# Optimization experiments

Hardware: AMD Instinct MI355X
Metric: run time of the kernel (lower is better)

## Reference

```python
import jax, jax.numpy as jnp
import numpy as np

EPS = 1e-12  # matches torch F.normalize eps


def setup_inputs() -> dict:
    key = jax.random.key(0)
    k1, k2, k3 = jax.random.split(key, 3)
    N, C, H, W, K = 16, 1024, 32, 32, 32
    x = jax.random.normal(k1, (N, C, H, W), dtype=jnp.float32)
    # 1x1 conv weight (K, C, 1, 1) stored as (K, C)
    conv_w = jax.random.normal(k2, (K, C), dtype=jnp.float32) * 0.02
    centroids = jax.random.uniform(k3, (K, C), dtype=jnp.float32)
    return {"x": x, "conv_w": conv_w, "centroids": centroids}


def _l2norm(v, axis):
    return v / jnp.maximum(jnp.linalg.norm(v, axis=axis, keepdims=True), EPS)


def reference(x, conv_w, centroids):
    N, C, H, W = x.shape
    K = centroids.shape[0]
    # normalize_input: L2 over channel dim
    x = _l2norm(x, axis=1)
    xf = x.reshape(N, C, H * W)                      # (N, C, P)
    # 1x1 conv == per-pixel matmul -> (N, K, P)
    logits = jnp.einsum('kc,ncp->nkp', conv_w, xf)
    a = jax.nn.softmax(logits, axis=1)               # softmax over clusters
    # sum_p a[n,k,p] * (x[n,:,p] - centroids[k,:])
    # == (a @ x^T) - (sum_p a) * centroids  (two GEMMs, no (N,K,C,P) blowup)
    vlad = jnp.einsum('nkp,ncp->nkc', a, xf) - a.sum(-1)[:, :, None] * centroids[None]
    vlad = _l2norm(vlad, axis=2)                     # intra-cluster L2 norm
    vlad = vlad.reshape(N, K * C)
    vlad = _l2norm(vlad, axis=1)                     # global L2 norm
    return vlad
```

## Files before the change

kernel.cpp:

```cpp
#include <hip/hip_runtime.h>

#define NB   16
#define CC   1024
#define PP   1024
#define KK   32
#define EPSF 1e-12f

typedef __attribute__((ext_vector_type(8))) short  bf16x8;
typedef __attribute__((ext_vector_type(4))) float  f32x4;

__device__ __forceinline__ float bf2f(unsigned short u) {
    union { unsigned int i; float f; } v; v.i = ((unsigned int)u) << 16; return v.f;
}
__device__ __forceinline__ unsigned short f2bf(float f) {
    union { float f; unsigned int i; } v; v.f = f;
    return (unsigned short)((v.i + 0x7fffu + ((v.i >> 16) & 1u)) >> 16);
}

template <typename T> struct IO;
template <> struct IO<float> {
    static __device__ __forceinline__ float ld(const float* p) { return *p; }
    static __device__ __forceinline__ f32x4 ld4(const float* p) { return *(const f32x4*)p; }
    static __device__ __forceinline__ void st4(float* p, f32x4 v) { *(f32x4*)p = v; }
};
template <> struct IO<unsigned short> {
    static __device__ __forceinline__ float ld(const unsigned short* p) { return bf2f(*p); }
    static __device__ __forceinline__ f32x4 ld4(const unsigned short* p) {
        const ushort4 u = *(const ushort4*)p;
        f32x4 r; r[0] = bf2f(u.x); r[1] = bf2f(u.y); r[2] = bf2f(u.z); r[3] = bf2f(u.w);
        return r;
    }
    static __device__ __forceinline__ void st4(unsigned short* p, f32x4 v) {
        ushort4 u;
        u.x = f2bf(v[0]); u.y = f2bf(v[1]); u.z = f2bf(v[2]); u.w = f2bf(v[3]);
        *(ushort4*)p = u;
    }
};

__device__ __forceinline__ void wg_sync_fast() {
    asm volatile("s_waitcnt lgkmcnt(0)" ::: "memory");
    __builtin_amdgcn_s_barrier();
    asm volatile("" ::: "memory");
}

struct __align__(16) AttnSmem {
    unsigned short xT[2][64][72];
    unsigned short Wl[2][32][72];
    float red[16][64];
    float rn[64];
};

template <typename T>
__device__ __forceinline__ void attn_body(const T* __restrict__ x,
                                          const T* __restrict__ w,
                                          AttnSmem& sm,
                                          float* __restrict__ rnorm_ws,
                                          unsigned short* __restrict__ attn_g,
                                          float* __restrict__ asum_p) {
    const int b = blockIdx.x, t = threadIdx.x;
    const int n = b >> 4, pt = b & 15, p0 = pt * 64;
    const int lane = t & 63, wv = t >> 6;
    const int quad = lane >> 4, l15 = lane & 15;
    const int i = t >> 4;
    const int j = t & 15;
    const int wk = t >> 3;
    const int wcoff = (t & 7) * 8;
    const size_t xb = (size_t)n * CC * PP + p0;

    float ssq_t[4] = {0.f, 0.f, 0.f, 0.f};
    f32x4 acc0 = {0.f, 0.f, 0.f, 0.f}, acc1 = {0.f, 0.f, 0.f, 0.f};

    f32x4 xr[4]; f32x4 wr[2];
    #pragma unroll
    for (int r = 0; r < 4; ++r)
        xr[r] = IO<T>::ld4(&x[xb + (size_t)(4 * i + r) * PP + 4 * j]);
    wr[0] = IO<T>::ld4(&w[wk * CC + wcoff]);
    wr[1] = IO<T>::ld4(&w[wk * CC + wcoff + 4]);

    #pragma unroll
    for (int ch = 0; ch < 16; ++ch) {
        const int buf = ch & 1;
        #pragma unroll
        for (int jj = 0; jj < 4; ++jj) {
            ssq_t[jj] += xr[0][jj] * xr[0][jj] + xr[1][jj] * xr[1][jj]
                       + xr[2][jj] * xr[2][jj] + xr[3][jj] * xr[3][jj];
            ushort4 u;
            u.x = f2bf(xr[0][jj]); u.y = f2bf(xr[1][jj]);
            u.z = f2bf(xr[2][jj]); u.w = f2bf(xr[3][jj]);
            *(ushort4*)&sm.xT[buf][4 * j + jj][4 * i] = u;
        }
        {
            ushort4 u0, u1;
            u0.x = f2bf(wr[0][0]); u0.y = f2bf(wr[0][1]);
            u0.z = f2bf(wr[0][2]); u0.w = f2bf(wr[0][3]);
            u1.x = f2bf(wr[1][0]); u1.y = f2bf(wr[1][1]);
            u1.z = f2bf(wr[1][2]); u1.w = f2bf(wr[1][3]);
            *(ushort4*)&sm.Wl[buf][wk][wcoff]     = u0;
            *(ushort4*)&sm.Wl[buf][wk][wcoff + 4] = u1;
        }
        if (ch < 15) {
            const int c0 = (ch + 1) * 64;
            #pragma unroll
            for (int r = 0; r < 4; ++r)
                xr[r] = IO<T>::ld4(&x[xb + (size_t)(c0 + 4 * i + r) * PP + 4 * j]);
            wr[0] = IO<T>::ld4(&w[wk * CC + c0 + wcoff]);
            wr[1] = IO<T>::ld4(&w[wk * CC + c0 + wcoff + 4]);
        }
        wg_sync_fast();
        #pragma unroll
        for (int ks = 0; ks < 2; ++ks) {
            const bf16x8 bv  = *(const bf16x8*)&sm.xT[buf][wv * 16 + l15][ks * 32 + quad * 8];
            const bf16x8 a0  = *(const bf16x8*)&sm.Wl[buf][l15][ks * 32 + quad * 8];
            const bf16x8 a1  = *(const bf16x8*)&sm.Wl[buf][16 + l15][ks * 32 + quad * 8];
            acc0 = __builtin_amdgcn_mfma_f32_16x16x32_bf16(a0, bv, acc0, 0, 0, 0);
            acc1 = __builtin_amdgcn_mfma_f32_16x16x32_bf16(a1, bv, acc1, 0, 0, 0);
        }
    }
    #pragma unroll
    for (int jj = 0; jj < 4; ++jj) sm.red[i][4 * j + jj] = ssq_t[jj];
    __syncthreads();
    if (t < 64) {
        float ss = 0.f;
        #pragma unroll
        for (int g = 0; g < 16; ++g) ss += sm.red[g][t];
        const float rr = 1.0f / fmaxf(sqrtf(ss), EPSF);
        sm.rn[t] = rr;
        rnorm_ws[n * PP + p0 + t] = rr;
    }
    __syncthreads();
    {
        const float rr = sm.rn[wv * 16 + l15];
        float l[8];
        #pragma unroll
        for (int reg = 0; reg < 4; ++reg) { l[reg] = acc0[reg] * rr; l[4 + reg] = acc1[reg] * rr; }
        float mx = l[0];
        #pragma unroll
        for (int q = 1; q < 8; ++q) mx = fmaxf(mx, l[q]);
        mx = fmaxf(mx, __shfl_xor(mx, 16, 64));
        mx = fmaxf(mx, __shfl_xor(mx, 32, 64));
        float e[8], sum = 0.f;
        #pragma unroll
        for (int q = 0; q < 8; ++q) { e[q] = expf(l[q] - mx); sum += e[q]; }
        sum += __shfl_xor(sum, 16, 64);
        sum += __shfl_xor(sum, 32, 64);
        const float inv = 1.0f / sum;
        #pragma unroll
        for (int reg = 0; reg < 4; ++reg) {
            sm.Wl[0][quad * 4 + reg][wv * 16 + l15]      = f2bf(e[reg] * inv);
            sm.Wl[0][16 + quad * 4 + reg][wv * 16 + l15] = f2bf(e[4 + reg] * inv);
        }
    }
    __syncthreads();
    {
        const int k = t >> 3, po = (t & 7) * 8;
        const ushort4 u0 = *(const ushort4*)&sm.Wl[0][k][po];
        const ushort4 u1 = *(const ushort4*)&sm.Wl[0][k][po + 4];
        *(ushort4*)&attn_g[((size_t)n * KK + k) * PP + p0 + po]     = u0;
        *(ushort4*)&attn_g[((size_t)n * KK + k) * PP + p0 + po + 4] = u1;
        float s = bf2f(u0.x) + bf2f(u0.y) + bf2f(u0.z) + bf2f(u0.w)
                + bf2f(u1.x) + bf2f(u1.y) + bf2f(u1.z) + bf2f(u1.w);
        s += __shfl_xor(s, 1, 64);
        s += __shfl_xor(s, 2, 64);
        s += __shfl_xor(s, 4, 64);
        if ((t & 7) == 0) asum_p[(n * 16 + pt) * KK + k] = s;
    }
}

__global__ __launch_bounds__(256) void k_attn(const void* __restrict__ xv,
                                              const void* __restrict__ wv,
                                              int* __restrict__ flag,
                                              float* __restrict__ rnorm_ws,
                                              unsigned short* __restrict__ attn_g,
                                              float* __restrict__ asum_p) {
    __shared__ AttnSmem sm;
    __shared__ int s_bad;
    const int t = threadIdx.x;
    if (t == 0) s_bad = 0;
    __syncthreads();
    {
        const unsigned short* xu = (const unsigned short*)xv;
        int bad = 0;
        for (int ii = t; ii < 4096; ii += 256)
            if (((xu[ii] >> 7) & 0xFFu) > 0x9Fu) bad = 1;
        if (bad) atomicOr(&s_bad, 1);
    }
    __syncthreads();
    const int f = s_bad;
    if (blockIdx.x == 0 && t == 0) flag[0] = f;
    if (f) attn_body<float>((const float*)xv, (const float*)wv, sm, rnorm_ws, attn_g, asum_p);
    else   attn_body<unsigned short>((const unsigned short*)xv, (const unsigned short*)wv,
                                     sm, rnorm_ws, attn_g, asum_p);
}

struct VladSmem { float asum[32]; float ssq[32]; };

template <typename T>
__device__ __forceinline__ void vlad_body(const T* __restrict__ x,
                                          const T* __restrict__ cent, VladSmem& sm,
                                          const float* __restrict__ rnorm_ws,
                                          const unsigned short* __restrict__ attn_g,
                                          const float* __restrict__ asum_p,
                                          float* __restrict__ vlad,
                                          float* __restrict__ ssqnk_p) {
    const int b = blockIdx.x, t = threadIdx.x;
    const int n = b >> 5, ct = b & 31;
    const int lane = t & 63, wvi = t >> 6;
    const int quad = lane >> 4, l15 = lane & 15;
    const int mt = wvi & 1, nt = wvi >> 1;
    const int krow = mt * 16 + l15;
    const int crow = ct * 32 + nt * 16 + l15;
    if (t < 32) {
        float s = 0.f;
        #pragma unroll
        for (int ps = 0; ps < 16; ++ps) s += asum_p[(n * 16 + ps) * KK + t];
        sm.asum[t] = s;
        sm.ssq[t] = 0.f;
    }
    __syncthreads();
    const unsigned short* apq = attn_g + ((size_t)n * KK + krow) * PP + quad * 8;
    const T* xp = x + (size_t)n * CC * PP + (size_t)crow * PP + quad * 8;
    const float* rp = rnorm_ws + n * PP + quad * 8;
    f32x4 acc = {0.f, 0.f, 0.f, 0.f};
    bf16x8 avq[4]; f32x4 xq0[4], xq1[4], rq0[4], rq1[4];
    #pragma unroll
    for (int ii = 0; ii < 4; ++ii) {
        const int o = ii * 32;
        avq[ii] = *(const bf16x8*)&apq[o];
        xq0[ii] = IO<T>::ld4(&xp[o]); xq1[ii] = IO<T>::ld4(&xp[o + 4]);
        rq0[ii] = *(const f32x4*)&rp[o]; rq1[ii] = *(const f32x4*)&rp[o + 4];
    }
    #pragma unroll
    for (int st = 0; st < 32; ++st) {
        const int sl = st & 3;
        bf16x8 bv;
        #pragma unroll
        for (int jj = 0; jj < 4; ++jj) {
            bv[jj]     = (short)f2bf(xq0[sl][jj] * rq0[sl][jj]);
            bv[4 + jj] = (short)f2bf(xq1[sl][jj] * rq1[sl][jj]);
        }
        acc = __builtin_amdgcn_mfma_f32_16x16x32_bf16(avq[sl], bv, acc, 0, 0, 0);
        if (st + 4 < 32) {
            const int o = (st + 4) * 32;
            avq[sl] = *(const bf16x8*)&apq[o];
            xq0[sl] = IO<T>::ld4(&xp[o]); xq1[sl] = IO<T>::ld4(&xp[o + 4]);
            rq0[sl] = *(const f32x4*)&rp[o]; rq1[sl] = *(const f32x4*)&rp[o + 4];
        }
    }
    #pragma unroll
    for (int reg = 0; reg < 4; ++reg) {
        const int kk = mt * 16 + quad * 4 + reg;
        const float A = sm.asum[kk];
        const float v = acc[reg] - A * IO<T>::ld(&cent[kk * CC + crow]);
        vlad[((size_t)n * KK + kk) * CC + crow] = v;
        float sq = v * v;
        sq += __shfl_xor(sq, 1, 64);
        sq += __shfl_xor(sq, 2, 64);
        sq += __shfl_xor(sq, 4, 64);
        sq += __shfl_xor(sq, 8, 64);
        if (l15 == 0) atomicAdd(&sm.ssq[kk], sq);
    }
    __syncthreads();
    if (t < 32) ssqnk_p[(n * 32 + ct) * KK + t] = sm.ssq[t];
}

__global__ __launch_bounds__(256) void k_vlad(const void* __restrict__ xv,
                                              const void* __restrict__ centv,
                                              const int* __restrict__ flag,
                                              const float* __restrict__ rnorm_ws,
                                              const unsigned short* __restrict__ attn_g,
                                              const float* __restrict__ asum_p,
                                              float* __restrict__ vlad,
                                              float* __restrict__ ssqnk_p) {
    __shared__ VladSmem sm;
    if (*flag) vlad_body<float>((const float*)xv, (const float*)centv, sm, rnorm_ws,
                                attn_g, asum_p, vlad, ssqnk_p);
    else       vlad_body<unsigned short>((const unsigned short*)xv, (const unsigned short*)centv,
                                         sm, rnorm_ws, attn_g, asum_p, vlad, ssqnk_p);
}

struct OutSmem { float ssq[32]; float rint[32]; float rg; };

template <typename T>
__device__ __forceinline__ void out_body(const float* __restrict__ vlad,
                                         const float* __restrict__ ssqnk_p,
                                         OutSmem& sm, T* __restrict__ out) {
    const int b = blockIdx.x, t = threadIdx.x;
    const int n = b >> 5, k = b & 31;
    if (t < 32) {
        float s = 0.f;
        #pragma unroll
        for (int ct = 0; ct < 32; ++ct) s += ssqnk_p[(n * 32 + ct) * KK + t];
        sm.ssq[t] = s;
    }
    __syncthreads();
    if (t < 64) {
        const float s = (t < 32) ? sm.ssq[t] : 0.f;
        const float rr = 1.0f / fmaxf(sqrtf(s), EPSF);
        float gg = s * rr * rr;
        #pragma unroll
        for (int off = 32; off > 0; off >>= 1) gg += __shfl_down(gg, off, 64);
        if (t == 0) sm.rg = 1.0f / fmaxf(sqrtf(gg), EPSF);
        if (t < 32) sm.rint[t] = rr;
    }
    __syncthreads();
    const float f = sm.rint[k] * sm.rg;
    const size_t ob = ((size_t)n * KK + k) * CC + 4 * t;
    f32x4 v = *(const f32x4*)&vlad[ob];
    v[0] *= f; v[1] *= f; v[2] *= f; v[3] *= f;
    IO<T>::st4(&out[ob], v);
}

__global__ __launch_bounds__(256) void k_out(const float* __restrict__ vlad,
                                             const float* __restrict__ ssqnk_p,
                                             const int* __restrict__ flag,
                                             void* __restrict__ outv) {
    __shared__ OutSmem sm;
    if (*flag) out_body<float>(vlad, ssqnk_p, sm, (float*)outv);
    else       out_body<unsigned short>(vlad, ssqnk_p, sm, (unsigned short*)outv);
}

extern "C" void kernel_launch(void* const* d_in, const int* in_sizes, int n_in,
                              void* d_out, int out_size, void* d_ws, size_t ws_size,
                              hipStream_t stream) {
    const void* x    = d_in[0];
    const void* w    = d_in[1];
    const void* cent = d_in[2];

    float* ws       = (float*)d_ws;
    float* rnorm_ws = ws;
    float* asum_p   = rnorm_ws + NB * PP;
    float* ssqnk_p  = asum_p + NB * 16 * KK;
    float* vlad     = ssqnk_p + NB * 32 * KK;
    int*   flag     = (int*)(vlad + (size_t)NB * KK * CC);
    unsigned short* attn_g = (unsigned short*)(flag + 4);

    k_attn<<<NB * 16, 256, 0, stream>>>(x, w, flag, rnorm_ws, attn_g, asum_p);
    k_vlad<<<NB * 32, 256, 0, stream>>>(x, cent, flag, rnorm_ws, attn_g, asum_p,
                                        vlad, ssqnk_p);
    k_out<<<NB * KK, 256, 0, stream>>>(vlad, ssqnk_p, flag, d_out);
}
```

Baseline: 133.0 us.

## Fold pixel inverse norm into attention weights and halve attention pixel tile

The per-pixel inverse L2 norm is now multiplied into the stored bf16 attention values, so the VLAD GEMM no longer loads a norm array or scales x per element, and the rnorm workspace is removed. The attention kernel now uses 32-pixel tiles with 128-channel chunks and one MFMA accumulator per wave, giving twice as many blocks. Softmax moves to a shared-memory layout whose buffers are unioned with the GEMM staging buffers. The soft-assignment sums are now taken from unrounded fp32 probabilities, and folding the norm before bf16 rounding changes the rounding slightly.

```diff
diff --git a/kernel.cpp b/kernel.cpp
--- a/kernel.cpp
+++ b/kernel.cpp
@@ -44,132 +44,148 @@
 }
 
 struct __align__(16) AttnSmem {
-    unsigned short xT[2][64][72];
-    unsigned short Wl[2][32][72];
-    float red[16][64];
-    float rn[64];
+    union {
+        struct {
+            unsigned short xT[2][32][136];
+            unsigned short Wl[2][32][136];
+        } m;
+        struct {
+            float red[32][32];
+            float lg[32][33];
+            float rn[32];
+            float asq[4][32];
+            unsigned short at[32][33];
+        } e;
+    } u;
 };
 
 template <typename T>
 __device__ __forceinline__ void attn_body(const T* __restrict__ x,
                                           const T* __restrict__ w,
                                           AttnSmem& sm,
-                                          float* __restrict__ rnorm_ws,
                                           unsigned short* __restrict__ attn_g,
                                           float* __restrict__ asum_p) {
     const int b = blockIdx.x, t = threadIdx.x;
-    const int n = b >> 4, pt = b & 15, p0 = pt * 64;
+    const int n = b >> 5, pt = b & 31, p0 = pt * 32;
     const int lane = t & 63, wv = t >> 6;
     const int quad = lane >> 4, l15 = lane & 15;
-    const int i = t >> 4;
-    const int j = t & 15;
+    const int khalf = wv >> 1, phalf = wv & 1;
+    const int ci = t >> 3;
+    const int pj = t & 7;
     const int wk = t >> 3;
-    const int wcoff = (t & 7) * 8;
+    const int wc = (t & 7) * 16;
     const size_t xb = (size_t)n * CC * PP + p0;
 
-    float ssq_t[4] = {0.f, 0.f, 0.f, 0.f};
-    f32x4 acc0 = {0.f, 0.f, 0.f, 0.f}, acc1 = {0.f, 0.f, 0.f, 0.f};
-
-    f32x4 xr[4]; f32x4 wr[2];
-    #pragma unroll
-    for (int r = 0; r < 4; ++r)
-        xr[r] = IO<T>::ld4(&x[xb + (size_t)(4 * i + r) * PP + 4 * j]);
-    wr[0] = IO<T>::ld4(&w[wk * CC + wcoff]);
-    wr[1] = IO<T>::ld4(&w[wk * CC + wcoff + 4]);
-
-    #pragma unroll
-    for (int ch = 0; ch < 16; ++ch) {
+    float ss[4] = {0.f, 0.f, 0.f, 0.f};
+    f32x4 acc = {0.f, 0.f, 0.f, 0.f};
+
+    f32x4 xr[4], wr[4];
+    #pragma unroll
+    for (int r = 0; r < 4; ++r) {
+        xr[r] = IO<T>::ld4(&x[xb + (size_t)(4 * ci + r) * PP + 4 * pj]);
+        wr[r] = IO<T>::ld4(&w[wk * CC + wc + 4 * r]);
+    }
+
+    #pragma unroll
+    for (int ch = 0; ch < 8; ++ch) {
         const int buf = ch & 1;
         #pragma unroll
         for (int jj = 0; jj < 4; ++jj) {
-            ssq_t[jj] += xr[0][jj] * xr[0][jj] + xr[1][jj] * xr[1][jj]
-                       + xr[2][jj] * xr[2][jj] + xr[3][jj] * xr[3][jj];
+            ss[jj] += xr[0][jj] * xr[0][jj] + xr[1][jj] * xr[1][jj]
+                    + xr[2][jj] * xr[2][jj] + xr[3][jj] * xr[3][jj];
             ushort4 u;
             u.x = f2bf(xr[0][jj]); u.y = f2bf(xr[1][jj]);
             u.z = f2bf(xr[2][jj]); u.w = f2bf(xr[3][jj]);
-            *(ushort4*)&sm.xT[buf][4 * j + jj][4 * i] = u;
-        }
-        {
-            ushort4 u0, u1;
-            u0.x = f2bf(wr[0][0]); u0.y = f2bf(wr[0][1]);
-            u0.z = f2bf(wr[0][2]); u0.w = f2bf(wr[0][3]);
-            u1.x = f2bf(wr[1][0]); u1.y = f2bf(wr[1][1]);
-            u1.z = f2bf(wr[1][2]); u1.w = f2bf(wr[1][3]);
-            *(ushort4*)&sm.Wl[buf][wk][wcoff]     = u0;
-            *(ushort4*)&sm.Wl[buf][wk][wcoff + 4] = u1;
-        }
-        if (ch < 15) {
-            const int c0 = (ch + 1) * 64;
+            *(ushort4*)&sm.u.m.xT[buf][4 * pj + jj][4 * ci] = u;
+        }
+        #pragma unroll
+        for (int r = 0; r < 4; ++r) {
+            ushort4 u;
+            u.x = f2bf(wr[r][0]); u.y = f2bf(wr[r][1]);
+            u.z = f2bf(wr[r][2]); u.w = f2bf(wr[r][3]);
+            *(ushort4*)&sm.u.m.Wl[buf][wk][wc + 4 * r] = u;
+        }
+        if (ch < 7) {
+            const int c0 = (ch + 1) * 128;
             #pragma unroll
-            for (int r = 0; r < 4; ++r)
-                xr[r] = IO<T>::ld4(&x[xb + (size_t)(c0 + 4 * i + r) * PP + 4 * j]);
-            wr[0] = IO<T>::ld4(&w[wk * CC + c0 + wcoff]);
-            wr[1] = IO<T>::ld4(&w[wk * CC + c0 + wcoff + 4]);
+            for (int r = 0; r < 4; ++r) {
+                xr[r] = IO<T>::ld4(&x[xb + (size_t)(c0 + 4 * ci + r) * PP + 4 * pj]);
+                wr[r] = IO<T>::ld4(&w[wk * CC + c0 + wc + 4 * r]);
+            }
         }
         wg_sync_fast();
         #pragma unroll
-        for (int ks = 0; ks < 2; ++ks) {
-            const bf16x8 bv  = *(const bf16x8*)&sm.xT[buf][wv * 16 + l15][ks * 32 + quad * 8];
-            const bf16x8 a0  = *(const bf16x8*)&sm.Wl[buf][l15][ks * 32 + quad * 8];
-            const bf16x8 a1  = *(const bf16x8*)&sm.Wl[buf][16 + l15][ks * 32 + quad * 8];
-            acc0 = __builtin_amdgcn_mfma_f32_16x16x32_bf16(a0, bv, acc0, 0, 0, 0);
-            acc1 = __builtin_amdgcn_mfma_f32_16x16x32_bf16(a1, bv, acc1, 0, 0, 0);
-        }
-    }
-    #pragma unroll
-    for (int jj = 0; jj < 4; ++jj) sm.red[i][4 * j + jj] = ssq_t[jj];
-    __syncthreads();
-    if (t < 64) {
-        float ss = 0.f;
-        #pragma unroll
-        for (int g = 0; g < 16; ++g) ss += sm.red[g][t];
-        const float rr = 1.0f / fmaxf(sqrtf(ss), EPSF);
-        sm.rn[t] = rr;
-        rnorm_ws[n * PP + p0 + t] = rr;
+        for (int ks = 0; ks < 4; ++ks) {
+            const bf16x8 av = *(const bf16x8*)&sm.u.m.Wl[buf][khalf * 16 + l15][ks * 32 + quad * 8];
+            const bf16x8 bv = *(const bf16x8*)&sm.u.m.xT[buf][phalf * 16 + l15][ks * 32 + quad * 8];
+            acc = __builtin_amdgcn_mfma_f32_16x16x32_bf16(av, bv, acc, 0, 0, 0);
+        }
+    }
+    __syncthreads();
+
+    #pragma unroll
+    for (int jj = 0; jj < 4; ++jj) sm.u.e.red[ci][4 * pj + jj] = ss[jj];
+    #pragma unroll
+    for (int reg = 0; reg < 4; ++reg)
+        sm.u.e.lg[phalf * 16 + l15][khalf * 16 + quad * 4 + reg] = acc[reg];
+    __syncthreads();
+    if (t < 32) {
+        float s = 0.f;
+        #pragma unroll
+        for (int g = 0; g < 32; ++g) s += sm.u.e.red[g][t];
+        sm.u.e.rn[t] = 1.0f / fmaxf(sqrtf(s), EPSF);
     }
     __syncthreads();
     {
-        const float rr = sm.rn[wv * 16 + l15];
-        float l[8];
-        #pragma unroll
-        for (int reg = 0; reg < 4; ++reg) { l[reg] = acc0[reg] * rr; l[4 + reg] = acc1[reg] * rr; }
-        float mx = l[0];
-        #pragma unroll
-        for (int q = 1; q < 8; ++q) mx = fmaxf(mx, l[q]);
-        mx = fmaxf(mx, __shfl_xor(mx, 16, 64));
-        mx = fmaxf(mx, __shfl_xor(mx, 32, 64));
-        float e[8], sum = 0.f;
-        #pragma unroll
-        for (int q = 0; q < 8; ++q) { e[q] = expf(l[q] - mx); sum += e[q]; }
-        sum += __shfl_xor(sum, 16, 64);
-        sum += __shfl_xor(sum, 32, 64);
+        const int p = t >> 3, kg = (t & 7) * 4;
+        const float rr = sm.u.e.rn[p];
+        float l[4];
+        #pragma unroll
+        for (int q = 0; q < 4; ++q) l[q] = sm.u.e.lg[p][kg + q] * rr;
+        float mx = fmaxf(fmaxf(l[0], l[1]), fmaxf(l[2], l[3]));
+        mx = fmaxf(mx, __shfl_xor(mx, 1, 64));
+        mx = fmaxf(mx, __shfl_xor(mx, 2, 64));
+        mx = fmaxf(mx, __shfl_xor(mx, 4, 64));
+        float e[4], sum = 0.f;
+        #pragma unroll
+        for (int q = 0; q < 4; ++q) { e[q] = expf(l[q] - mx); sum += e[q]; }
+        sum += __shfl_xor(sum, 1, 64);
+        sum += __shfl_xor(sum, 2, 64);
+        sum += __shfl_xor(sum, 4, 64);
         const float inv = 1.0f / sum;
-        #pragma unroll
-        for (int reg = 0; reg < 4; ++reg) {
-            sm.Wl[0][quad * 4 + reg][wv * 16 + l15]      = f2bf(e[reg] * inv);
-            sm.Wl[0][16 + quad * 4 + reg][wv * 16 + l15] = f2bf(e[4 + reg] * inv);
-        }
-    }
-    __syncthreads();
+        float a[4];
+        #pragma unroll
+        for (int q = 0; q < 4; ++q) {
+            a[q] = e[q] * inv;
+            sm.u.e.at[kg + q][p] = f2bf(a[q] * rr);
+        }
+        #pragma unroll
+        for (int q = 0; q < 4; ++q) {
+            a[q] += __shfl_xor(a[q], 8, 64);
+            a[q] += __shfl_xor(a[q], 16, 64);
+            a[q] += __shfl_xor(a[q], 32, 64);
+        }
+        if ((lane >> 3) == 0) {
+            #pragma unroll
+            for (int q = 0; q < 4; ++q) sm.u.e.asq[wv][kg + q] = a[q];
+        }
+    }
+    __syncthreads();
+    if (t < 32)
+        asum_p[(n * 32 + pt) * KK + t]
+            = sm.u.e.asq[0][t] + sm.u.e.asq[1][t] + sm.u.e.asq[2][t] + sm.u.e.asq[3][t];
     {
-        const int k = t >> 3, po = (t & 7) * 8;
-        const ushort4 u0 = *(const ushort4*)&sm.Wl[0][k][po];
-        const ushort4 u1 = *(const ushort4*)&sm.Wl[0][k][po + 4];
-        *(ushort4*)&attn_g[((size_t)n * KK + k) * PP + p0 + po]     = u0;
-        *(ushort4*)&attn_g[((size_t)n * KK + k) * PP + p0 + po + 4] = u1;
-        float s = bf2f(u0.x) + bf2f(u0.y) + bf2f(u0.z) + bf2f(u0.w)
-                + bf2f(u1.x) + bf2f(u1.y) + bf2f(u1.z) + bf2f(u1.w);
-        s += __shfl_xor(s, 1, 64);
-        s += __shfl_xor(s, 2, 64);
-        s += __shfl_xor(s, 4, 64);
-        if ((t & 7) == 0) asum_p[(n * 16 + pt) * KK + k] = s;
+        const int k = t >> 3, po = (t & 7) * 4;
+        ushort4 u;
+        u.x = sm.u.e.at[k][po];     u.y = sm.u.e.at[k][po + 1];
+        u.z = sm.u.e.at[k][po + 2]; u.w = sm.u.e.at[k][po + 3];
+        *(ushort4*)&attn_g[((size_t)n * KK + k) * PP + p0 + po] = u;
     }
 }
 
 __global__ __launch_bounds__(256) void k_attn(const void* __restrict__ xv,
                                               const void* __restrict__ wv,
                                               int* __restrict__ flag,
-                                              float* __restrict__ rnorm_ws,
                                               unsigned short* __restrict__ attn_g,
                                               float* __restrict__ asum_p) {
     __shared__ AttnSmem sm;
@@ -187,9 +203,9 @@
     __syncthreads();
     const int f = s_bad;
     if (blockIdx.x == 0 && t == 0) flag[0] = f;
-    if (f) attn_body<float>((const float*)xv, (const float*)wv, sm, rnorm_ws, attn_g, asum_p);
+    if (f) attn_body<float>((const float*)xv, (const float*)wv, sm, attn_g, asum_p);
     else   attn_body<unsigned short>((const unsigned short*)xv, (const unsigned short*)wv,
-                                     sm, rnorm_ws, attn_g, asum_p);
+                                     sm, attn_g, asum_p);
 }
 
 struct VladSmem { float asum[32]; float ssq[32]; };
@@ -197,7 +213,6 @@
 template <typename T>
 __device__ __forceinline__ void vlad_body(const T* __restrict__ x,
                                           const T* __restrict__ cent, VladSmem& sm,
-                                          const float* __restrict__ rnorm_ws,
                                           const unsigned short* __restrict__ attn_g,
                                           const float* __restrict__ asum_p,
                                           float* __restrict__ vlad,
@@ -212,22 +227,20 @@
     if (t < 32) {
         float s = 0.f;
         #pragma unroll
-        for (int ps = 0; ps < 16; ++ps) s += asum_p[(n * 16 + ps) * KK + t];
+        for (int ps = 0; ps < 32; ++ps) s += asum_p[(n * 32 + ps) * KK + t];
         sm.asum[t] = s;
         sm.ssq[t] = 0.f;
     }
     __syncthreads();
     const unsigned short* apq = attn_g + ((size_t)n * KK + krow) * PP + quad * 8;
     const T* xp = x + (size_t)n * CC * PP + (size_t)crow * PP + quad * 8;
-    const float* rp = rnorm_ws + n * PP + quad * 8;
     f32x4 acc = {0.f, 0.f, 0.f, 0.f};
-    bf16x8 avq[4]; f32x4 xq0[4], xq1[4], rq0[4], rq1[4];
+    bf16x8 avq[4]; f32x4 xq0[4], xq1[4];
     #pragma unroll
     for (int ii = 0; ii < 4; ++ii) {
         const int o = ii * 32;
         avq[ii] = *(const bf16x8*)&apq[o];
         xq0[ii] = IO<T>::ld4(&xp[o]); xq1[ii] = IO<T>::ld4(&xp[o + 4]);
-        rq0[ii] = *(const f32x4*)&rp[o]; rq1[ii] = *(const f32x4*)&rp[o + 4];
     }
     #pragma unroll
     for (int st = 0; st < 32; ++st) {
@@ -235,15 +248,14 @@
         bf16x8 bv;
         #pragma unroll
         for (int jj = 0; jj < 4; ++jj) {
-            bv[jj]     = (short)f2bf(xq0[sl][jj] * rq0[sl][jj]);
-            bv[4 + jj] = (short)f2bf(xq1[sl][jj] * rq1[sl][jj]);
+            bv[jj]     = (short)f2bf(xq0[sl][jj]);
+            bv[4 + jj] = (short)f2bf(xq1[sl][jj]);
         }
         acc = __builtin_amdgcn_mfma_f32_16x16x32_bf16(avq[sl], bv, acc, 0, 0, 0);
         if (st + 4 < 32) {
             const int o = (st + 4) * 32;
             avq[sl] = *(const bf16x8*)&apq[o];
             xq0[sl] = IO<T>::ld4(&xp[o]); xq1[sl] = IO<T>::ld4(&xp[o + 4]);
-            rq0[sl] = *(const f32x4*)&rp[o]; rq1[sl] = *(const f32x4*)&rp[o + 4];
         }
     }
     #pragma unroll
@@ -266,16 +278,15 @@
 __global__ __launch_bounds__(256) void k_vlad(const void* __restrict__ xv,
                                               const void* __restrict__ centv,
                                               const int* __restrict__ flag,
-                                              const float* __restrict__ rnorm_ws,
                                               const unsigned short* __restrict__ attn_g,
                                               const float* __restrict__ asum_p,
                                               float* __restrict__ vlad,
                                               float* __restrict__ ssqnk_p) {
     __shared__ VladSmem sm;
-    if (*flag) vlad_body<float>((const float*)xv, (const float*)centv, sm, rnorm_ws,
+    if (*flag) vlad_body<float>((const float*)xv, (const float*)centv, sm,
                                 attn_g, asum_p, vlad, ssqnk_p);
     else       vlad_body<unsigned short>((const unsigned short*)xv, (const unsigned short*)centv,
-                                         sm, rnorm_ws, attn_g, asum_p, vlad, ssqnk_p);
+                                         sm, attn_g, asum_p, vlad, ssqnk_p);
 }
 
 struct OutSmem { float ssq[32]; float rint[32]; float rg; };
@@ -326,16 +337,14 @@
     const void* w    = d_in[1];
     const void* cent = d_in[2];
 
-    float* ws       = (float*)d_ws;
-    float* rnorm_ws = ws;
-    float* asum_p   = rnorm_ws + NB * PP;
-    float* ssqnk_p  = asum_p + NB * 16 * KK;
-    float* vlad     = ssqnk_p + NB * 32 * KK;
-    int*   flag     = (int*)(vlad + (size_t)NB * KK * CC);
+    float* ws      = (float*)d_ws;
+    float* asum_p  = ws;
+    float* ssqnk_p = asum_p + NB * 32 * KK;
+    float* vlad    = ssqnk_p + NB * 32 * KK;
+    int*   flag    = (int*)(vlad + (size_t)NB * KK * CC);
     unsigned short* attn_g = (unsigned short*)(flag + 4);
 
-    k_attn<<<NB * 16, 256, 0, stream>>>(x, w, flag, rnorm_ws, attn_g, asum_p);
-    k_vlad<<<NB * 32, 256, 0, stream>>>(x, cent, flag, rnorm_ws, attn_g, asum_p,
-                                        vlad, ssqnk_p);
+    k_attn<<<NB * 32, 256, 0, stream>>>(x, w, flag, attn_g, asum_p);
+    k_vlad<<<NB * 32, 256, 0, stream>>>(x, cent, flag, attn_g, asum_p, vlad, ssqnk_p);
     k_out<<<NB * KK, 256, 0, stream>>>(vlad, ssqnk_p, flag, d_out);
 }
```

Result: faster. 130.0 us (-2.2%).
